# Kernel optimization log

Measured on AMD Instinct MI355X. Metric: run time of the kernel, lower is better.

Reference implementation:

```python
import jax, jax.numpy as jnp
import numpy as np

NUM_HEADS = 16
LN_EPS = 1e-5


def setup_inputs() -> dict:
    key = jax.random.key(0)
    ks = jax.random.split(key, 5)
    B, S, E = 4, 1024, 1024
    x = jax.random.normal(ks[0], (B, S, E), dtype=jnp.float32)
    # Linear weights stored torch-style [out, in]; scaled for stable softmax
    Wq = jax.random.normal(ks[1], (E, E), dtype=jnp.float32) * (E ** -0.5)
    Wk = jax.random.normal(ks[2], (E, E), dtype=jnp.float32) * (E ** -0.5)
    Wv = jax.random.normal(ks[3], (E, E), dtype=jnp.float32) * (E ** -0.5)
    Wo = jax.random.normal(ks[4], (E, E), dtype=jnp.float32) * (E ** -0.5)
    gamma = jnp.ones((E,), dtype=jnp.float32)
    beta = jnp.zeros((E,), dtype=jnp.float32)
    return {"x": x, "Wq": Wq, "Wk": Wk, "Wv": Wv, "Wo": Wo, "gamma": gamma, "beta": beta}


def reference(x, Wq, Wk, Wv, Wo, gamma, beta):
    B, S, E = x.shape
    H = NUM_HEADS
    D = E // H
    scale = 1.0 / (D ** 0.5)

    q = x @ Wq.T                      # [B,S,E]
    k = (x @ Wk.T) * scale            # [B,S,E]
    v = x @ Wv.T                      # [B,S,E]

    qh = q.reshape(B, S, H, D)
    kh = k.reshape(B, S, H, D)
    qk = jnp.einsum('bthd,bshd->bhts', qh, kh)        # [B,H,T,S]

    causal = jnp.tril(jnp.ones((S, S), dtype=bool))   # mask==0 -> -inf
    qk = jnp.where(causal, qk, -jnp.inf)
    attn = jax.nn.softmax(qk, axis=-1)                # [B,H,T,S]

    # Faithful to torch.unflatten(v, dim=2, sizes=[-1, num_heads]):
    # heads are the LAST axis of the value split (transposed vs q/k).
    vh = v.reshape(B, S, D, H)                        # [B,S,D,H]
    # einsum 'kjlm,kmij->kiml': out[b,t,h,d] = sum_s vh[b,s,d,h]*attn[b,h,t,s]
    qkv = jnp.einsum('bsdh,bhts->bthd', vh, attn)     # [B,T,H,D]
    qkv = qkv.reshape(B, S, E)

    # LayerNorm over last dim
    mu = jnp.mean(qkv, axis=-1, keepdims=True)
    var = jnp.mean(jnp.square(qkv - mu), axis=-1, keepdims=True)
    ln = (qkv - mu) * jax.lax.rsqrt(var + LN_EPS) * gamma + beta

    return ln @ Wo.T
```

## Files before the change

### kernel.cpp

```cpp
#include <hip/hip_runtime.h>
#include <stdint.h>


using bf16x8 = __attribute__((ext_vector_type(8))) short;
using f32x4  = __attribute__((ext_vector_type(4))) float;
using u16x8  = __attribute__((ext_vector_type(8))) unsigned short;

#define AS1 __attribute__((address_space(1)))
#define AS3 __attribute__((address_space(3)))

__device__ __forceinline__ void gload16(const void* g, void* l) {
  __builtin_amdgcn_global_load_lds((const AS1 uint32_t*)g, (AS3 uint32_t*)l, 16, 0, 0);
}

__device__ __forceinline__ unsigned short f2bf(float f) {
  union { float f; uint32_t u; } v; v.f = f;
  uint32_t u = v.u + 0x7fffu + ((v.u >> 16) & 1u);
  return (unsigned short)(u >> 16);
}
__device__ __forceinline__ float bf2f(unsigned short h) {
  union { uint32_t u; float f; } v; v.u = ((uint32_t)h) << 16;
  return v.f;
}

__global__ __launch_bounds__(256) void cvt_all(const float* __restrict__ x,
                                               const float* __restrict__ Wq,
                                               const float* __restrict__ Wk,
                                               const float* __restrict__ Wv,
                                               const float* __restrict__ Wo,
                                               unsigned short* __restrict__ xb,
                                               unsigned short* __restrict__ wcat,
                                               unsigned short* __restrict__ wob) {
  int i = (int)blockIdx.x * 256 + (int)threadIdx.x;
  const float* src; unsigned short* dst; int off; float scale = 1.0f;
  if (i < 1048576)      { src = x;  dst = xb;             off = i; }
  else if (i < 1310720) { src = Wq; dst = wcat;           off = i - 1048576; }
  else if (i < 1572864) { src = Wk; dst = wcat + 1048576; off = i - 1310720; scale = 0.125f; }
  else if (i < 1835008) { src = Wv; dst = wcat + 2097152; off = i - 1572864; }
  else                  { src = Wo; dst = wob;            off = i - 1835008; }
  float4 v = reinterpret_cast<const float4*>(src)[off];
  ushort4 o;
  o.x = f2bf(v.x * scale);
  o.y = f2bf(v.y * scale);
  o.z = f2bf(v.z * scale);
  o.w = f2bf(v.w * scale);
  reinterpret_cast<ushort4*>(dst)[off] = o;
}

template<int OUTF32, int TM>
__global__ __launch_bounds__(256, 3) void gemm_bt(const unsigned short* __restrict__ A,
                                                  const unsigned short* __restrict__ B,
                                                  void* __restrict__ Cv,
                                                  int N, int K) {
  constexpr int MI = TM / 32;
  __shared__ __align__(16) unsigned short lA[2][TM * 32];
  __shared__ __align__(16) unsigned short lB[2][128 * 32];
  const int tn_cnt = N >> 7;
  const int nwg = gridDim.x;
  int bid = (int)blockIdx.x;
  int bid2 = (bid & 7) * (nwg >> 3) + (bid >> 3);
  int tm = bid2 / tn_cnt, tn = bid2 % tn_cnt;
  int t = (int)threadIdx.x;
  int w = t >> 6, lane = t & 63, lr = lane & 15, hi = lane >> 4;
  int wr = w >> 1, wc = w & 1;

  auto stage = [&](int kt, int buf) {
#pragma unroll
    for (int j = 0; j < TM / 64; ++j) {
      int ch = j * 256 + t;
      int row = ch >> 2, slot = ch & 3;
      gload16(A + (size_t)(tm * TM + row) * K + kt * 32 + ((slot ^ (row & 3)) << 3),
              (char*)lA[buf] + j * 4096 + w * 1024);
    }
#pragma unroll
    for (int j = 0; j < 2; ++j) {
      int ch = j * 256 + t;
      int row = ch >> 2, slot = ch & 3;
      gload16(B + (size_t)(tn * 128 + row) * K + kt * 32 + ((slot ^ (row & 3)) << 3),
              (char*)lB[buf] + j * 4096 + w * 1024);
    }
  };

  f32x4 acc[MI][4] = {};
  stage(0, 0);
  __syncthreads();
  const int NT = K >> 5;
  for (int kt = 0; kt < NT; ++kt) {
    int cur = kt & 1;
    if (kt + 1 < NT) stage(kt + 1, cur ^ 1);
    const char* pa = (const char*)lA[cur];
    const char* pb = (const char*)lB[cur];
    bf16x8 af[MI], bfr[4];
#pragma unroll
    for (int mi = 0; mi < MI; ++mi) {
      int row = wr * (TM / 2) + mi * 16 + lr;
      int slot = hi ^ (row & 3);
      af[mi] = *reinterpret_cast<const bf16x8*>(pa + row * 64 + slot * 16);
    }
#pragma unroll
    for (int ni = 0; ni < 4; ++ni) {
      int row = wc * 64 + ni * 16 + lr;
      int slot = hi ^ (row & 3);
      bfr[ni] = *reinterpret_cast<const bf16x8*>(pb + row * 64 + slot * 16);
    }
#pragma unroll
    for (int mi = 0; mi < MI; ++mi)
#pragma unroll
      for (int ni = 0; ni < 4; ++ni)
        acc[mi][ni] = __builtin_amdgcn_mfma_f32_16x16x32_bf16(af[mi], bfr[ni], acc[mi][ni], 0, 0, 0);
    __syncthreads();
  }
#pragma unroll
  for (int mi = 0; mi < MI; ++mi) {
#pragma unroll
    for (int r = 0; r < 4; ++r) {
      size_t row = (size_t)(tm * TM + wr * (TM / 2) + mi * 16 + hi * 4 + r);
#pragma unroll
      for (int ni = 0; ni < 4; ++ni) {
        int col = tn * 128 + wc * 64 + ni * 16 + lr;
        float v = acc[mi][ni][r];
        if (OUTF32) reinterpret_cast<float*>(Cv)[row * N + col] = v;
        else        reinterpret_cast<unsigned short*>(Cv)[row * N + col] = f2bf(v);
      }
    }
  }
}

__global__ __launch_bounds__(256) void vrepack(const unsigned short* __restrict__ QKV,
                                               unsigned short* __restrict__ VhT) {
  __shared__ __align__(16) unsigned short lT[64 * 72];
  int st = (int)blockIdx.x;
  int ct = (int)blockIdx.y;
  int b  = (int)blockIdx.z;
  int t = (int)threadIdx.x;
#pragma unroll
  for (int i = 0; i < 2; ++i) {
    int c = i * 256 + t;
    int row = c >> 3, ch = c & 7;
    u16x8 v = *reinterpret_cast<const u16x8*>(
        QKV + (size_t)(b * 1024 + st * 64 + row) * 3072 + 2048 + ct * 64 + ch * 8);
    *reinterpret_cast<u16x8*>(&lT[row * 72 + ch * 8]) = v;
  }
  __syncthreads();
#pragma unroll
  for (int i = 0; i < 2; ++i) {
    int c2 = i * 256 + t;
    int cl = c2 >> 3, ch = c2 & 7;
    int h = cl & 15;
    int d = ct * 4 + (cl >> 4);
    u16x8 v;
#pragma unroll
    for (int j = 0; j < 8; ++j) v[j] = lT[(ch * 8 + j) * 72 + cl];
    *reinterpret_cast<u16x8*>(
        VhT + (size_t)((b * 16 + h) * 64 + d) * 1024 + st * 64 + ch * 8) = v;
  }
}

__global__ __launch_bounds__(256, 2) void attn_fwd(const unsigned short* __restrict__ QKV,
                                                   const unsigned short* __restrict__ VhT,
                                                   unsigned short* __restrict__ Out) {
  __shared__ __align__(16) unsigned short lK[2][64 * 64];
  __shared__ __align__(16) unsigned short lV[2][64 * 64];
  __shared__ __align__(16) unsigned short lQP[64 * 64];
  int bid = (int)blockIdx.x;
  int bh = bid >> 3, j = bid & 7;
  int b = bh >> 4, h = bh & 15;
  int t = (int)threadIdx.x;
  int w = t >> 6, lane = t & 63, lr = lane & 15, hi = lane >> 4;
  (void)lane;

  auto stageKV = [&](int kb, int buf) {
#pragma unroll
    for (int i = 0; i < 2; ++i) {
      int c = i * 256 + t;
      int row = c >> 3, slot = c & 7;
      gload16(QKV + (size_t)(b * 1024 + kb * 64 + row) * 3072 + 1024 + h * 64 + ((slot ^ (row & 7)) << 3),
              (char*)lK + buf * 8192 + i * 4096 + w * 1024);
    }
#pragma unroll
    for (int i = 0; i < 2; ++i) {
      int c = i * 256 + t;
      int row = c >> 3, slot = c & 7;
      gload16(VhT + (size_t)(bh * 64 + row) * 1024 + kb * 64 + ((slot ^ (row & 7)) << 3),
              (char*)lV + buf * 8192 + i * 4096 + w * 1024);
    }
  };

#pragma unroll 1
  for (int pass = 0; pass < 2; ++pass) {
    int qt = pass ? (15 - j) : j;
#pragma unroll
    for (int i = 0; i < 2; ++i) {
      int c = i * 256 + t;
      int row = c >> 3, slot = c & 7;
      gload16(QKV + (size_t)(b * 1024 + qt * 64 + row) * 3072 + h * 64 + ((slot ^ (row & 7)) << 3),
              (char*)lQP + i * 4096 + w * 1024);
    }
    stageKV(0, 0);
    __syncthreads();

    bf16x8 qfr[2];
#pragma unroll
    for (int kc = 0; kc < 2; ++kc) {
      int row = w * 16 + lr;
      int slot = (kc * 4 + hi) ^ (row & 7);
      qfr[kc] = *reinterpret_cast<const bf16x8*>((const char*)lQP + row * 128 + slot * 16);
    }
    int qbase = qt * 64 + w * 16;
    f32x4 o[4] = {};
    float mrun[4], lpart[4];
#pragma unroll
    for (int r = 0; r < 4; ++r) { mrun[r] = -1e30f; lpart[r] = 0.f; }

    int nkb = qt + 1;
    for (int kb = 0; kb < nkb; ++kb) {
      int cur = kb & 1;
      if (kb + 1 < nkb) stageKV(kb + 1, cur ^ 1);
      const char* kbuf = (const char*)lK + cur * 8192;
      const char* vbuf = (const char*)lV + cur * 8192;
      bf16x8 kfr[4][2];
#pragma unroll
      for (int nf = 0; nf < 4; ++nf)
#pragma unroll
        for (int kc = 0; kc < 2; ++kc) {
          int row = nf * 16 + lr;
          int slot = (kc * 4 + hi) ^ (row & 7);
          kfr[nf][kc] = *reinterpret_cast<const bf16x8*>(kbuf + row * 128 + slot * 16);
        }
      f32x4 s[4] = {};
#pragma unroll
      for (int nf = 0; nf < 4; ++nf)
#pragma unroll
        for (int kc = 0; kc < 2; ++kc)
          s[nf] = __builtin_amdgcn_mfma_f32_16x16x32_bf16(qfr[kc], kfr[nf][kc], s[nf], 0, 0, 0);
      bf16x8 vfr[4][2];
#pragma unroll
      for (int df = 0; df < 4; ++df)
#pragma unroll
        for (int kc = 0; kc < 2; ++kc) {
          int row = df * 16 + lr;
          int slot = (kc * 4 + hi) ^ (row & 7);
          vfr[df][kc] = *reinterpret_cast<const bf16x8*>(vbuf + row * 128 + slot * 16);
        }
      if (kb == qt) {
#pragma unroll
        for (int nf = 0; nf < 4; ++nf)
#pragma unroll
          for (int r = 0; r < 4; ++r) {
            int q = qbase + hi * 4 + r;
            int kv = kb * 64 + nf * 16 + lr;
            if (kv > q) s[nf][r] = -1e30f;
          }
      }
      float rm[4];
#pragma unroll
      for (int r = 0; r < 4; ++r)
        rm[r] = fmaxf(fmaxf(s[0][r], s[1][r]), fmaxf(s[2][r], s[3][r]));
#pragma unroll
      for (int r = 0; r < 4; ++r) {
        rm[r] = fmaxf(rm[r], __shfl_xor(rm[r], 1));
        rm[r] = fmaxf(rm[r], __shfl_xor(rm[r], 2));
        rm[r] = fmaxf(rm[r], __shfl_xor(rm[r], 4));
        rm[r] = fmaxf(rm[r], __shfl_xor(rm[r], 8));
      }
#pragma unroll
      for (int r = 0; r < 4; ++r) {
        float mn = fmaxf(mrun[r], rm[r]);
        float al = __expf(mrun[r] - mn);
        mrun[r] = mn;
        float ps = 0.f;
#pragma unroll
        for (int nf = 0; nf < 4; ++nf) {
          float p = __expf(s[nf][r] - mn);
          s[nf][r] = p;
          ps += p;
        }
        lpart[r] = lpart[r] * al + ps;
#pragma unroll
        for (int df = 0; df < 4; ++df) o[df][r] *= al;
      }
      char* pb = (char*)lQP + w * 2048;
#pragma unroll
      for (int nf = 0; nf < 4; ++nf)
#pragma unroll
        for (int r = 0; r < 4; ++r) {
          int rp = hi * 4 + r;
          int col = nf * 16 + lr;
          int slot = (col >> 3) ^ (rp & 7);
          *reinterpret_cast<unsigned short*>(pb + rp * 128 + slot * 16 + (col & 7) * 2) =
              f2bf(s[nf][r]);
        }
      asm volatile("s_waitcnt lgkmcnt(0)" ::: "memory");
      __builtin_amdgcn_sched_barrier(0);
      bf16x8 pfr[2];
#pragma unroll
      for (int kc = 0; kc < 2; ++kc) {
        int row = lr;
        int slot = (kc * 4 + hi) ^ (row & 7);
        pfr[kc] = *reinterpret_cast<const bf16x8*>(pb + row * 128 + slot * 16);
      }
#pragma unroll
      for (int df = 0; df < 4; ++df)
#pragma unroll
        for (int kc = 0; kc < 2; ++kc)
          o[df] = __builtin_amdgcn_mfma_f32_16x16x32_bf16(pfr[kc], vfr[df][kc], o[df], 0, 0, 0);
      __syncthreads();
    }

#pragma unroll
    for (int r = 0; r < 4; ++r) {
      float l = lpart[r];
      l += __shfl_xor(l, 1);
      l += __shfl_xor(l, 2);
      l += __shfl_xor(l, 4);
      l += __shfl_xor(l, 8);
      float inv = 1.0f / l;
      int qrow = qbase + hi * 4 + r;
#pragma unroll
      for (int df = 0; df < 4; ++df)
        Out[(size_t)(b * 1024 + qrow) * 1024 + h * 64 + df * 16 + lr] = f2bf(o[df][r] * inv);
    }
    __syncthreads();
  }
}

__global__ __launch_bounds__(256) void lnorm(const unsigned short* __restrict__ X,
                                             unsigned short* __restrict__ Y,
                                             const float* __restrict__ gamma,
                                             const float* __restrict__ beta) {
  int rowi = (int)blockIdx.x * 4 + ((int)threadIdx.x >> 6);
  int lane = (int)threadIdx.x & 63;
  const unsigned short* row = X + (size_t)rowi * 1024;
  u16x8 v0 = reinterpret_cast<const u16x8*>(row)[lane];
  u16x8 v1 = reinterpret_cast<const u16x8*>(row)[lane + 64];
  float f0[8], f1[8];
  float s = 0.f, sq = 0.f;
#pragma unroll
  for (int j = 0; j < 8; ++j) {
    f0[j] = bf2f(v0[j]); f1[j] = bf2f(v1[j]);
    s  += f0[j] + f1[j];
    sq += f0[j] * f0[j] + f1[j] * f1[j];
  }
#pragma unroll
  for (int m = 1; m <= 32; m <<= 1) { s += __shfl_xor(s, m); sq += __shfl_xor(sq, m); }
  float mean = s * (1.0f / 1024.0f);
  float var  = sq * (1.0f / 1024.0f) - mean * mean;
  float rstd = rsqrtf(var + 1e-5f);
  int c0 = lane * 8, c1 = 512 + lane * 8;
  u16x8 o0, o1;
#pragma unroll
  for (int j = 0; j < 8; ++j) {
    o0[j] = f2bf((f0[j] - mean) * rstd * gamma[c0 + j] + beta[c0 + j]);
    o1[j] = f2bf((f1[j] - mean) * rstd * gamma[c1 + j] + beta[c1 + j]);
  }
  reinterpret_cast<u16x8*>(Y + (size_t)rowi * 1024)[lane]      = o0;
  reinterpret_cast<u16x8*>(Y + (size_t)rowi * 1024)[lane + 64] = o1;
}

extern "C" void kernel_launch(void* const* d_in, const int* in_sizes, int n_in,
                              void* d_out, int out_size, void* d_ws, size_t ws_size,
                              hipStream_t stream) {
  (void)in_sizes; (void)n_in; (void)out_size; (void)ws_size;
  const float* x     = (const float*)d_in[0];
  const float* Wq    = (const float*)d_in[1];
  const float* Wk    = (const float*)d_in[2];
  const float* Wv    = (const float*)d_in[3];
  const float* Wo    = (const float*)d_in[4];
  const float* gamma = (const float*)d_in[5];
  const float* beta  = (const float*)d_in[6];
  char* ws = (char*)d_ws;
  unsigned short* xb   = (unsigned short*)(ws);
  unsigned short* wcat = (unsigned short*)(ws + (8u  << 20));
  unsigned short* wob  = (unsigned short*)(ws + (14u << 20));
  unsigned short* qkv  = (unsigned short*)(ws + (16u << 20));
  unsigned short* vht  = (unsigned short*)(ws + (40u << 20));
  unsigned short* att  = (unsigned short*)(ws + (48u << 20));
  unsigned short* lnb  = (unsigned short*)(ws + (56u << 20));

  cvt_all<<<8192, 256, 0, stream>>>(x, Wq, Wk, Wv, Wo, xb, wcat, wob);
  gemm_bt<0, 128><<<768, 256, 0, stream>>>(xb, wcat, qkv, 3072, 1024);
  vrepack<<<dim3(16, 16, 4), 256, 0, stream>>>(qkv, vht);
  attn_fwd<<<512, 256, 0, stream>>>(qkv, vht, att);
  lnorm<<<1024, 256, 0, stream>>>(att, lnb, gamma, beta);
  gemm_bt<1, 64><<<512, 256, 0, stream>>>(lnb, wob, (void*)d_out, 1024, 1024);
}
```

Baseline: 183.1 us.

## Fuse V transpose into QKV GEMM epilogue and widen attention KV tiles

The QKV GEMM epilogue now writes the V columns directly in the head-transposed VhT layout, which removes the separate vrepack kernel and its extra read and write pass over V. Separately, the attention kernel now processes 128-key blocks instead of 64, halving the number of loop iterations and barriers per query tile. The larger blocks double the LDS footprint for K/V/P and increase register pressure (s[8], kfr[8][2], vfr[4][4]), which may lower occupancy. They also waste masked work on the diagonal block.

```diff
diff --git a/kernel.cpp b/kernel.cpp
--- a/kernel.cpp
+++ b/kernel.cpp
@@ -47,10 +47,11 @@
   reinterpret_cast<ushort4*>(dst)[off] = o;
 }
 
-template<int OUTF32, int TM>
+template<int OUTF32, int TM, int FUSEV>
 __global__ __launch_bounds__(256, 3) void gemm_bt(const unsigned short* __restrict__ A,
                                                   const unsigned short* __restrict__ B,
                                                   void* __restrict__ Cv,
+                                                  unsigned short* __restrict__ Vht,
                                                   int N, int K) {
   constexpr int MI = TM / 32;
   __shared__ __align__(16) unsigned short lA[2][TM * 32];
@@ -110,58 +111,47 @@
         acc[mi][ni] = __builtin_amdgcn_mfma_f32_16x16x32_bf16(af[mi], bfr[ni], acc[mi][ni], 0, 0, 0);
     __syncthreads();
   }
-#pragma unroll
-  for (int mi = 0; mi < MI; ++mi) {
-#pragma unroll
-    for (int r = 0; r < 4; ++r) {
-      size_t row = (size_t)(tm * TM + wr * (TM / 2) + mi * 16 + hi * 4 + r);
+  if (FUSEV && tn >= 16) {
+#pragma unroll
+    for (int mi = 0; mi < MI; ++mi) {
+      size_t row0 = (size_t)(tm * TM + wr * (TM / 2) + mi * 16 + hi * 4);
+      int bb = (int)(row0 >> 10), ss = (int)(row0 & 1023);
 #pragma unroll
       for (int ni = 0; ni < 4; ++ni) {
-        int col = tn * 128 + wc * 64 + ni * 16 + lr;
-        float v = acc[mi][ni][r];
-        if (OUTF32) reinterpret_cast<float*>(Cv)[row * N + col] = v;
-        else        reinterpret_cast<unsigned short*>(Cv)[row * N + col] = f2bf(v);
-      }
-    }
-  }
-}
-
-__global__ __launch_bounds__(256) void vrepack(const unsigned short* __restrict__ QKV,
-                                               unsigned short* __restrict__ VhT) {
-  __shared__ __align__(16) unsigned short lT[64 * 72];
-  int st = (int)blockIdx.x;
-  int ct = (int)blockIdx.y;
-  int b  = (int)blockIdx.z;
-  int t = (int)threadIdx.x;
-#pragma unroll
-  for (int i = 0; i < 2; ++i) {
-    int c = i * 256 + t;
-    int row = c >> 3, ch = c & 7;
-    u16x8 v = *reinterpret_cast<const u16x8*>(
-        QKV + (size_t)(b * 1024 + st * 64 + row) * 3072 + 2048 + ct * 64 + ch * 8);
-    *reinterpret_cast<u16x8*>(&lT[row * 72 + ch * 8]) = v;
-  }
-  __syncthreads();
-#pragma unroll
-  for (int i = 0; i < 2; ++i) {
-    int c2 = i * 256 + t;
-    int cl = c2 >> 3, ch = c2 & 7;
-    int h = cl & 15;
-    int d = ct * 4 + (cl >> 4);
-    u16x8 v;
-#pragma unroll
-    for (int j = 0; j < 8; ++j) v[j] = lT[(ch * 8 + j) * 72 + cl];
-    *reinterpret_cast<u16x8*>(
-        VhT + (size_t)((b * 16 + h) * 64 + d) * 1024 + st * 64 + ch * 8) = v;
+        int cv0 = (tn - 16) * 128 + wc * 64 + ni * 16;
+        int d = cv0 >> 4;
+        ushort4 pk;
+        pk.x = f2bf(acc[mi][ni][0]);
+        pk.y = f2bf(acc[mi][ni][1]);
+        pk.z = f2bf(acc[mi][ni][2]);
+        pk.w = f2bf(acc[mi][ni][3]);
+        *reinterpret_cast<ushort4*>(Vht + ((size_t)(bb * 16 + lr) * 64 + d) * 1024 + ss) = pk;
+      }
+    }
+  } else {
+#pragma unroll
+    for (int mi = 0; mi < MI; ++mi) {
+#pragma unroll
+      for (int r = 0; r < 4; ++r) {
+        size_t row = (size_t)(tm * TM + wr * (TM / 2) + mi * 16 + hi * 4 + r);
+#pragma unroll
+        for (int ni = 0; ni < 4; ++ni) {
+          int col = tn * 128 + wc * 64 + ni * 16 + lr;
+          float v = acc[mi][ni][r];
+          if (OUTF32) reinterpret_cast<float*>(Cv)[row * N + col] = v;
+          else        reinterpret_cast<unsigned short*>(Cv)[row * N + col] = f2bf(v);
+        }
+      }
+    }
   }
 }
 
 __global__ __launch_bounds__(256, 2) void attn_fwd(const unsigned short* __restrict__ QKV,
                                                    const unsigned short* __restrict__ VhT,
                                                    unsigned short* __restrict__ Out) {
-  __shared__ __align__(16) unsigned short lK[2][64 * 64];
-  __shared__ __align__(16) unsigned short lV[2][64 * 64];
-  __shared__ __align__(16) unsigned short lQP[64 * 64];
+  __shared__ __align__(16) unsigned short lK[2][128 * 64];
+  __shared__ __align__(16) unsigned short lV[2][64 * 128];
+  __shared__ __align__(16) unsigned short lQP[8192];
   int bid = (int)blockIdx.x;
   int bh = bid >> 3, j = bid & 7;
   int b = bh >> 4, h = bh & 15;
@@ -171,18 +161,18 @@
 
   auto stageKV = [&](int kb, int buf) {
 #pragma unroll
-    for (int i = 0; i < 2; ++i) {
+    for (int i = 0; i < 4; ++i) {
       int c = i * 256 + t;
       int row = c >> 3, slot = c & 7;
-      gload16(QKV + (size_t)(b * 1024 + kb * 64 + row) * 3072 + 1024 + h * 64 + ((slot ^ (row & 7)) << 3),
-              (char*)lK + buf * 8192 + i * 4096 + w * 1024);
-    }
-#pragma unroll
-    for (int i = 0; i < 2; ++i) {
+      gload16(QKV + (size_t)(b * 1024 + kb * 128 + row) * 3072 + 1024 + h * 64 + ((slot ^ (row & 7)) << 3),
+              (char*)lK[buf] + i * 4096 + w * 1024);
+    }
+#pragma unroll
+    for (int i = 0; i < 4; ++i) {
       int c = i * 256 + t;
-      int row = c >> 3, slot = c & 7;
-      gload16(VhT + (size_t)(bh * 64 + row) * 1024 + kb * 64 + ((slot ^ (row & 7)) << 3),
-              (char*)lV + buf * 8192 + i * 4096 + w * 1024);
+      int row = c >> 4, sl = c & 15;
+      gload16(VhT + (size_t)(bh * 64 + row) * 1024 + kb * 128 + ((sl ^ (row & 7)) << 3),
+              (char*)lV[buf] + i * 4096 + w * 1024);
     }
   };
 
@@ -212,50 +202,53 @@
 #pragma unroll
     for (int r = 0; r < 4; ++r) { mrun[r] = -1e30f; lpart[r] = 0.f; }
 
-    int nkb = qt + 1;
+    int nkb = (qt + 2) >> 1;
     for (int kb = 0; kb < nkb; ++kb) {
       int cur = kb & 1;
       if (kb + 1 < nkb) stageKV(kb + 1, cur ^ 1);
-      const char* kbuf = (const char*)lK + cur * 8192;
-      const char* vbuf = (const char*)lV + cur * 8192;
-      bf16x8 kfr[4][2];
-#pragma unroll
-      for (int nf = 0; nf < 4; ++nf)
+      const char* kbuf = (const char*)lK[cur];
+      const char* vbuf = (const char*)lV[cur];
+      bf16x8 kfr[8][2];
+#pragma unroll
+      for (int nf = 0; nf < 8; ++nf)
 #pragma unroll
         for (int kc = 0; kc < 2; ++kc) {
           int row = nf * 16 + lr;
           int slot = (kc * 4 + hi) ^ (row & 7);
           kfr[nf][kc] = *reinterpret_cast<const bf16x8*>(kbuf + row * 128 + slot * 16);
         }
-      f32x4 s[4] = {};
-#pragma unroll
-      for (int nf = 0; nf < 4; ++nf)
+      f32x4 s[8] = {};
+#pragma unroll
+      for (int nf = 0; nf < 8; ++nf)
 #pragma unroll
         for (int kc = 0; kc < 2; ++kc)
           s[nf] = __builtin_amdgcn_mfma_f32_16x16x32_bf16(qfr[kc], kfr[nf][kc], s[nf], 0, 0, 0);
-      bf16x8 vfr[4][2];
+      bf16x8 vfr[4][4];
 #pragma unroll
       for (int df = 0; df < 4; ++df)
 #pragma unroll
-        for (int kc = 0; kc < 2; ++kc) {
+        for (int kc = 0; kc < 4; ++kc) {
           int row = df * 16 + lr;
           int slot = (kc * 4 + hi) ^ (row & 7);
-          vfr[df][kc] = *reinterpret_cast<const bf16x8*>(vbuf + row * 128 + slot * 16);
-        }
-      if (kb == qt) {
-#pragma unroll
-        for (int nf = 0; nf < 4; ++nf)
+          vfr[df][kc] = *reinterpret_cast<const bf16x8*>(vbuf + row * 256 + slot * 16);
+        }
+      if (kb == nkb - 1) {
+#pragma unroll
+        for (int nf = 0; nf < 8; ++nf)
 #pragma unroll
           for (int r = 0; r < 4; ++r) {
             int q = qbase + hi * 4 + r;
-            int kv = kb * 64 + nf * 16 + lr;
+            int kv = kb * 128 + nf * 16 + lr;
             if (kv > q) s[nf][r] = -1e30f;
           }
       }
       float rm[4];
 #pragma unroll
-      for (int r = 0; r < 4; ++r)
-        rm[r] = fmaxf(fmaxf(s[0][r], s[1][r]), fmaxf(s[2][r], s[3][r]));
+      for (int r = 0; r < 4; ++r) {
+        float m0 = fmaxf(fmaxf(s[0][r], s[1][r]), fmaxf(s[2][r], s[3][r]));
+        float m1 = fmaxf(fmaxf(s[4][r], s[5][r]), fmaxf(s[6][r], s[7][r]));
+        rm[r] = fmaxf(m0, m1);
+      }
 #pragma unroll
       for (int r = 0; r < 4; ++r) {
         rm[r] = fmaxf(rm[r], __shfl_xor(rm[r], 1));
@@ -270,7 +263,7 @@
         mrun[r] = mn;
         float ps = 0.f;
 #pragma unroll
-        for (int nf = 0; nf < 4; ++nf) {
+        for (int nf = 0; nf < 8; ++nf) {
           float p = __expf(s[nf][r] - mn);
           s[nf][r] = p;
           ps += p;
@@ -279,30 +272,29 @@
 #pragma unroll
         for (int df = 0; df < 4; ++df) o[df][r] *= al;
       }
-      char* pb = (char*)lQP + w * 2048;
-#pragma unroll
-      for (int nf = 0; nf < 4; ++nf)
+      char* pb = (char*)lQP + w * 4096;
+#pragma unroll
+      for (int nf = 0; nf < 8; ++nf)
 #pragma unroll
         for (int r = 0; r < 4; ++r) {
           int rp = hi * 4 + r;
           int col = nf * 16 + lr;
           int slot = (col >> 3) ^ (rp & 7);
-          *reinterpret_cast<unsigned short*>(pb + rp * 128 + slot * 16 + (col & 7) * 2) =
+          *reinterpret_cast<unsigned short*>(pb + rp * 256 + slot * 16 + (col & 7) * 2) =
               f2bf(s[nf][r]);
         }
       asm volatile("s_waitcnt lgkmcnt(0)" ::: "memory");
       __builtin_amdgcn_sched_barrier(0);
-      bf16x8 pfr[2];
-#pragma unroll
-      for (int kc = 0; kc < 2; ++kc) {
-        int row = lr;
-        int slot = (kc * 4 + hi) ^ (row & 7);
-        pfr[kc] = *reinterpret_cast<const bf16x8*>(pb + row * 128 + slot * 16);
+      bf16x8 pfr[4];
+#pragma unroll
+      for (int kc = 0; kc < 4; ++kc) {
+        int slot = (kc * 4 + hi) ^ (lr & 7);
+        pfr[kc] = *reinterpret_cast<const bf16x8*>(pb + lr * 256 + slot * 16);
       }
 #pragma unroll
       for (int df = 0; df < 4; ++df)
 #pragma unroll
-        for (int kc = 0; kc < 2; ++kc)
+        for (int kc = 0; kc < 4; ++kc)
           o[df] = __builtin_amdgcn_mfma_f32_16x16x32_bf16(pfr[kc], vfr[df][kc], o[df], 0, 0, 0);
       __syncthreads();
     }
@@ -378,9 +370,8 @@
   unsigned short* lnb  = (unsigned short*)(ws + (56u << 20));
 
   cvt_all<<<8192, 256, 0, stream>>>(x, Wq, Wk, Wv, Wo, xb, wcat, wob);
-  gemm_bt<0, 128><<<768, 256, 0, stream>>>(xb, wcat, qkv, 3072, 1024);
-  vrepack<<<dim3(16, 16, 4), 256, 0, stream>>>(qkv, vht);
+  gemm_bt<0, 128, 1><<<768, 256, 0, stream>>>(xb, wcat, qkv, vht, 3072, 1024);
   attn_fwd<<<512, 256, 0, stream>>>(qkv, vht, att);
   lnorm<<<1024, 256, 0, stream>>>(att, lnb, gamma, beta);
-  gemm_bt<1, 64><<<512, 256, 0, stream>>>(lnb, wob, (void*)d_out, 1024, 1024);
-}
+  gemm_bt<1, 64, 0><<<512, 256, 0, stream>>>(lnb, wob, (void*)d_out, nullptr, 1024, 1024);
+}
```

Result: faster. 178.0 us (-2.8%).
